# Kernel optimization log

Measured on AMD Instinct MI355X. Metric: run time of the kernel, lower is better.

The kernel has to match this reference:

```python
import jax, jax.numpy as jnp
import numpy as np

INC, ICS = 32, 8      # in_caps, in_caps_size
ONC, OCS = 32, 16     # out_caps, out_caps_size
K, STRIDE, PAD = 3, 1, 0
ITERS = 3


def squash(t, axis=-1):
    sq = jnp.sum(t * t, axis=axis, keepdims=True)
    return (sq / (1.0 + sq)) * t / jnp.sqrt(sq)


def setup_inputs() -> dict:
    key = jax.random.key(0)
    k1, k2 = jax.random.split(key)
    x = jax.random.normal(k1, (4, INC * ICS, 14, 14), dtype=jnp.float32)
    # nn.Parameter(torch.randn(...)); scaled by 1/sqrt(ICS) for numerical sanity
    weight = jax.random.normal(k2, (ONC, INC * K * K, ICS, OCS), dtype=jnp.float32) * (1.0 / np.sqrt(ICS))
    return {"x": x, "weight": weight}


def reference(x, weight):
    B, C, H, W = x.shape
    OH = (H + 2 * PAD - K) // STRIDE + 1
    OW = (W + 2 * PAD - K) // STRIDE + 1
    # Tile2d: extract KxK patches -> (B, C*K*K, OH, OW), channel order (C, kh, kw)
    patches = jax.lax.conv_general_dilated_patches(
        x, (K, K), (STRIDE, STRIDE), padding=((PAD, PAD), (PAD, PAD)))
    # (B, INC, ICS, K*K, OH*OW) -> (B, OH*OW, K*K, INC, ICS) -> (N, KK*INC, ICS)
    tiles = patches.reshape(B, INC, ICS, K * K, OH * OW)
    tiles = tiles.transpose(0, 4, 3, 1, 2).reshape(B * OH * OW, K * K * INC, ICS)

    # priors: (ONC, N, KKI, OCS)  == x[None,:,:,None,:] @ W[:,None]
    priors = jnp.einsum('nki,okic->onkc', tiles, weight)

    # dynamic routing; logits broadcast over OCS in the original (identical math)
    N = B * OH * OW
    KKI = K * K * INC
    logits = jnp.zeros((ONC, N, KKI, 1), dtype=priors.dtype)
    outputs = None
    for i in range(ITERS):
        probs = jax.nn.softmax(logits, axis=2)              # over KKI routes
        outputs = squash(jnp.sum(probs * priors, axis=2, keepdims=True))  # (ONC,N,1,OCS)
        if i != ITERS - 1:
            logits = logits + jnp.sum(priors * outputs, axis=-1, keepdims=True)

    # (ONC, N, OCS) -> (N, ONC, OCS) -> (B, ONC*OCS, OH, OW)
    out = outputs[:, :, 0, :].transpose(1, 0, 2)
    out = out.reshape(B, OH, OW, ONC * OCS).transpose(0, 3, 1, 2)
    return out
```

## Files before the change

kernel.cpp:

```cpp
#include <hip/hip_runtime.h>

static constexpr int OHW = 12, NSP = 144;

__global__ void build_T(const float* __restrict__ x, float4* __restrict__ T4) {
    const int g = blockIdx.x * 256 + threadIdx.x;
    const int n = g / 576;
    const int q = g - n * 576;
    const int r = q << 2;
    const int k = r >> 3;
    const int i0 = r & 7;
    const int ic = k & 31;
    const int kk = k >> 5;
    const int kh = kk / 3, kw = kk - kh * 3;
    const int b = n / NSP;
    const int rm = n - b * NSP;
    const int oh = rm / OHW, ow = rm - oh * OHW;
    const float* xp = x + (size_t)(b * 256 + ic * 8 + i0) * 196
                        + (oh + kh) * 14 + (ow + kw);
    float4 v;
    v.x = xp[0];
    v.y = xp[196];
    v.z = xp[392];
    v.w = xp[588];
    T4[g] = v;
}

__device__ __forceinline__ void fma4(float4& a, float s, const float4& w) {
    a.x = fmaf(s, w.x, a.x);
    a.y = fmaf(s, w.y, a.y);
    a.z = fmaf(s, w.z, a.z);
    a.w = fmaf(s, w.w, a.w);
}

__device__ __forceinline__ float4 shfl_xor4(const float4& v, int m) {
    float4 r;
    r.x = __shfl_xor(v.x, m);
    r.y = __shfl_xor(v.y, m);
    r.z = __shfl_xor(v.z, m);
    r.w = __shfl_xor(v.w, m);
    return r;
}

__device__ __forceinline__ void do_j(const float4* __restrict__ T4,
                                     const float4* __restrict__ W4,
                                     float4* __restrict__ Pl,
                                     int o, int nbase, int k, int cg,
                                     int g_local, int lane) {
    float4 w[8];
    const float4* wp = W4 + (size_t)(o * 288 + k) * 32 + cg;
    #pragma unroll
    for (int i = 0; i < 8; ++i) w[i] = wp[i * 4];
    #pragma unroll
    for (int nn = 0; nn < 4; ++nn) {
        const float4* tp = T4 + (size_t)(nbase + nn) * 576 + k * 2;
        const float4 t0 = tp[0];
        const float4 t1 = tp[1];
        float4 a = make_float4(0.f, 0.f, 0.f, 0.f);
        fma4(a, t0.x, w[0]); fma4(a, t0.y, w[1]);
        fma4(a, t0.z, w[2]); fma4(a, t0.w, w[3]);
        fma4(a, t1.x, w[4]); fma4(a, t1.y, w[5]);
        fma4(a, t1.z, w[6]); fma4(a, t1.w, w[7]);
        Pl[nn * 576 + g_local * 64 + lane] = a;
    }
}

__global__ __launch_bounds__(256, 4)
void caps_main(const float4* __restrict__ T4, const float4* __restrict__ W4,
               float* __restrict__ out) {
    __shared__ float4 Pl[4 * 9 * 64];
    const int tid = threadIdx.x;
    const int o = blockIdx.y;
    const int nbase = blockIdx.x * 4;
    const int cg = tid & 3;
    const int kg = tid >> 2;
    const int wv = tid >> 6;
    const int lane = tid & 63;

    float4 P[18];

    #pragma unroll
    for (int j = 0; j < 5; ++j) {
        const int k = kg + 64 * j;
        const int g = wv + 4 * j;
        if (k < 288 && g < 9)
            do_j(T4, W4, Pl, o, nbase, k, cg, g, lane);
    }
    __syncthreads();
    #pragma unroll
    for (int jj = 0; jj < 9; ++jj)
        P[jj] = Pl[wv * 576 + jj * 64 + lane];
    __syncthreads();
    #pragma unroll
    for (int j = 0; j < 5; ++j) {
        const int k = kg + 64 * j;
        const int g = wv + 4 * j;
        if (k < 288 && g >= 9)
            do_j(T4, W4, Pl, o, nbase, k, cg, g - 9, lane);
    }
    __syncthreads();
    #pragma unroll
    for (int jj = 9; jj < 18; ++jj)
        P[jj] = Pl[wv * 576 + (jj - 9) * 64 + lane];

    float lj[18];
    #pragma unroll
    for (int jj = 0; jj < 18; ++jj) lj[jj] = 0.f;
    float4 vq = make_float4(0.f, 0.f, 0.f, 0.f);

    #pragma unroll
    for (int it = 0; it < 3; ++it) {
        float4 svU = make_float4(0.f, 0.f, 0.f, 0.f);
        float S;
        if (it == 0) {
            #pragma unroll
            for (int jj = 0; jj < 18; ++jj) {
                svU.x += P[jj].x; svU.y += P[jj].y;
                svU.z += P[jj].z; svU.w += P[jj].w;
            }
            #pragma unroll
            for (int m = 4; m < 64; m <<= 1) {
                const float4 t = shfl_xor4(svU, m);
                svU.x += t.x; svU.y += t.y; svU.z += t.z; svU.w += t.w;
            }
            S = 288.0f;
        } else {
            S = 0.f;
            #pragma unroll
            for (int jj = 0; jj < 18; ++jj) {
                const float e = __expf(lj[jj]);
                S += e;
                fma4(svU, e, P[jj]);
            }
            #pragma unroll
            for (int m = 4; m < 64; m <<= 1) {
                const float4 t = shfl_xor4(svU, m);
                svU.x += t.x; svU.y += t.y; svU.z += t.z; svU.w += t.w;
                S += __shfl_xor(S, m);
            }
        }
        const float invS = __frcp_rn(S);
        float4 s;
        s.x = svU.x * invS; s.y = svU.y * invS;
        s.z = svU.z * invS; s.w = svU.w * invS;
        float sq = s.x * s.x + s.y * s.y + s.z * s.z + s.w * s.w;
        sq += __shfl_xor(sq, 1);
        sq += __shfl_xor(sq, 2);
        const float scale = __fsqrt_rn(sq) / (1.0f + sq);
        vq.x = s.x * scale; vq.y = s.y * scale;
        vq.z = s.z * scale; vq.w = s.w * scale;

        if (it < 2) {
            #pragma unroll
            for (int jj = 0; jj < 18; ++jj) {
                float d = P[jj].x * vq.x + P[jj].y * vq.y +
                          P[jj].z * vq.z + P[jj].w * vq.w;
                d += __shfl_xor(d, 1);
                d += __shfl_xor(d, 2);
                lj[jj] += d;
            }
        }
    }

    if ((lane >> 2) == 0) {
        const int n = nbase + wv;
        const int b = n / NSP;
        const int rm = n - b * NSP;
        float* op = out + (size_t)(b * 512 + o * 16 + cg * 4) * NSP + rm;
        op[0 * NSP] = vq.x;
        op[1 * NSP] = vq.y;
        op[2 * NSP] = vq.z;
        op[3 * NSP] = vq.w;
    }
}

extern "C" void kernel_launch(void* const* d_in, const int* in_sizes, int n_in,
                              void* d_out, int out_size, void* d_ws, size_t ws_size,
                              hipStream_t stream) {
    const float* x  = (const float*)d_in[0];
    const float* wt = (const float*)d_in[1];
    float* out = (float*)d_out;
    float4* T4 = (float4*)d_ws;

    build_T<<<dim3(576 * 576 / 256), 256, 0, stream>>>(x, T4);
    caps_main<<<dim3(144, 32), 256, 0, stream>>>(T4, (const float4*)wt, out);
}
```

Baseline: 123.6 us.

## Fuse patch extraction into routing kernel, reading input directly

Drops the separate build_T kernel that materialised the im2col tile buffer in workspace. The main kernel now reads the four adjacent output-width positions straight from x with an unaligned 4-wide vector load per input channel and computes the priors from them. This removes one kernel launch and a full write and read of the tile buffer. In exchange it relies on the four positions in a block sharing a row (12 is divisible by 4) and on unaligned vector loads.

After: 130.9 us. +5.9%, slower.

```diff
diff --git a/kernel.cpp b/kernel.cpp
--- a/kernel.cpp
+++ b/kernel.cpp
@@ -2,28 +2,7 @@
 
 static constexpr int OHW = 12, NSP = 144;
 
-__global__ void build_T(const float* __restrict__ x, float4* __restrict__ T4) {
-    const int g = blockIdx.x * 256 + threadIdx.x;
-    const int n = g / 576;
-    const int q = g - n * 576;
-    const int r = q << 2;
-    const int k = r >> 3;
-    const int i0 = r & 7;
-    const int ic = k & 31;
-    const int kk = k >> 5;
-    const int kh = kk / 3, kw = kk - kh * 3;
-    const int b = n / NSP;
-    const int rm = n - b * NSP;
-    const int oh = rm / OHW, ow = rm - oh * OHW;
-    const float* xp = x + (size_t)(b * 256 + ic * 8 + i0) * 196
-                        + (oh + kh) * 14 + (ow + kw);
-    float4 v;
-    v.x = xp[0];
-    v.y = xp[196];
-    v.z = xp[392];
-    v.w = xp[588];
-    T4[g] = v;
-}
+typedef float float4a __attribute__((ext_vector_type(4), aligned(4)));
 
 __device__ __forceinline__ void fma4(float4& a, float s, const float4& w) {
     a.x = fmaf(s, w.x, a.x);
@@ -41,32 +20,44 @@
     return r;
 }
 
-__device__ __forceinline__ void do_j(const float4* __restrict__ T4,
+__device__ __forceinline__ void do_j(const float* __restrict__ xb,
                                      const float4* __restrict__ W4,
                                      float4* __restrict__ Pl,
-                                     int o, int nbase, int k, int cg,
+                                     int o, int k, int cg,
                                      int g_local, int lane) {
     float4 w[8];
     const float4* wp = W4 + (size_t)(o * 288 + k) * 32 + cg;
     #pragma unroll
     for (int i = 0; i < 8; ++i) w[i] = wp[i * 4];
+
+    const int ic = k & 31;
+    const int kk = k >> 5;
+    const int kh = (kk * 11) >> 5;
+    const int kw = kk - 3 * kh;
+    const float* xp = xb + ic * (8 * 196) + kh * 14 + kw;
+
+    float4a v[8];
     #pragma unroll
-    for (int nn = 0; nn < 4; ++nn) {
-        const float4* tp = T4 + (size_t)(nbase + nn) * 576 + k * 2;
-        const float4 t0 = tp[0];
-        const float4 t1 = tp[1];
-        float4 a = make_float4(0.f, 0.f, 0.f, 0.f);
-        fma4(a, t0.x, w[0]); fma4(a, t0.y, w[1]);
-        fma4(a, t0.z, w[2]); fma4(a, t0.w, w[3]);
-        fma4(a, t1.x, w[4]); fma4(a, t1.y, w[5]);
-        fma4(a, t1.z, w[6]); fma4(a, t1.w, w[7]);
-        Pl[nn * 576 + g_local * 64 + lane] = a;
+    for (int i = 0; i < 8; ++i) v[i] = *(const float4a*)(xp + i * 196);
+
+    float4 acc[4];
+    #pragma unroll
+    for (int nn = 0; nn < 4; ++nn) acc[nn] = make_float4(0.f, 0.f, 0.f, 0.f);
+    #pragma unroll
+    for (int i = 0; i < 8; ++i) {
+        fma4(acc[0], v[i].x, w[i]);
+        fma4(acc[1], v[i].y, w[i]);
+        fma4(acc[2], v[i].z, w[i]);
+        fma4(acc[3], v[i].w, w[i]);
     }
+    #pragma unroll
+    for (int nn = 0; nn < 4; ++nn)
+        Pl[nn * 576 + g_local * 64 + lane] = acc[nn];
 }
 
 __global__ __launch_bounds__(256, 4)
-void caps_main(const float4* __restrict__ T4, const float4* __restrict__ W4,
-               float* __restrict__ out) {
+void caps_fused(const float* __restrict__ x, const float4* __restrict__ W4,
+                float* __restrict__ out) {
     __shared__ float4 Pl[4 * 9 * 64];
     const int tid = threadIdx.x;
     const int o = blockIdx.y;
@@ -76,6 +67,12 @@
     const int wv = tid >> 6;
     const int lane = tid & 63;
 
+    const int b = nbase / NSP;
+    const int rm = nbase - b * NSP;
+    const int oh = rm / OHW;
+    const int ow0 = rm - oh * OHW;
+    const float* xb = x + (size_t)b * (256 * 196) + oh * 14 + ow0;
+
     float4 P[18];
 
     #pragma unroll
@@ -83,7 +80,7 @@
         const int k = kg + 64 * j;
         const int g = wv + 4 * j;
         if (k < 288 && g < 9)
-            do_j(T4, W4, Pl, o, nbase, k, cg, g, lane);
+            do_j(xb, W4, Pl, o, k, cg, g, lane);
     }
     __syncthreads();
     #pragma unroll
@@ -95,7 +92,7 @@
         const int k = kg + 64 * j;
         const int g = wv + 4 * j;
         if (k < 288 && g >= 9)
-            do_j(T4, W4, Pl, o, nbase, k, cg, g - 9, lane);
+            do_j(xb, W4, Pl, o, k, cg, g - 9, lane);
     }
     __syncthreads();
     #pragma unroll
@@ -162,10 +159,7 @@
     }
 
     if ((lane >> 2) == 0) {
-        const int n = nbase + wv;
-        const int b = n / NSP;
-        const int rm = n - b * NSP;
-        float* op = out + (size_t)(b * 512 + o * 16 + cg * 4) * NSP + rm;
+        float* op = out + (size_t)(b * 512 + o * 16 + cg * 4) * NSP + (rm + wv);
         op[0 * NSP] = vq.x;
         op[1 * NSP] = vq.y;
         op[2 * NSP] = vq.z;
@@ -179,8 +173,5 @@
     const float* x  = (const float*)d_in[0];
     const float* wt = (const float*)d_in[1];
     float* out = (float*)d_out;
-    float4* T4 = (float4*)d_ws;
-
-    build_T<<<dim3(576 * 576 / 256), 256, 0, stream>>>(x, T4);
-    caps_main<<<dim3(144, 32), 256, 0, stream>>>(T4, (const float4*)wt, out);
+    caps_fused<<<dim3(144, 32), 256, 0, stream>>>(x, (const float4*)wt, out);
 }
```

## Split routing across two waves per position with 512-thread blocks

Applied to the files above, without the earlier changes.

Each capsule block now uses 512 threads, and each spatial position is handled by two wavefronts. Each wavefront holds 9 of the 18 prior float4s per lane, which halves per-thread register pressure and raises the launch bounds occupancy target. Partial routing sums and softmax denominators are combined across the wave pair through shared memory, at the cost of extra __syncthreads per routing iteration. Prior computation is redistributed so the two halves are produced in two phases over the same shared buffer.

After: 148.9 us. +20.5%, slower.

```diff
diff --git a/kernel.cpp b/kernel.cpp
--- a/kernel.cpp
+++ b/kernel.cpp
@@ -32,6 +32,10 @@
     a.w = fmaf(s, w.w, a.w);
 }
 
+__device__ __forceinline__ void add4(float4& a, const float4& b) {
+    a.x += b.x; a.y += b.y; a.z += b.z; a.w += b.w;
+}
+
 __device__ __forceinline__ float4 shfl_xor4(const float4& v, int m) {
     float4 r;
     r.x = __shfl_xor(v.x, m);
@@ -64,7 +68,7 @@
     }
 }
 
-__global__ __launch_bounds__(256, 4)
+__global__ __launch_bounds__(512, 6)
 void caps_main(const float4* __restrict__ T4, const float4* __restrict__ W4,
                float* __restrict__ out) {
     __shared__ float4 Pl[4 * 9 * 64];
@@ -72,39 +76,46 @@
     const int o = blockIdx.y;
     const int nbase = blockIdx.x * 4;
     const int cg = tid & 3;
-    const int kg = tid >> 2;
+    const int lane = tid & 63;
+    const int kgp = lane >> 2;
     const int wv = tid >> 6;
-    const int lane = tid & 63;
+    const int nl = wv >> 1;
+    const int khf = wv & 1;
 
-    float4 P[18];
+    do_j(T4, W4, Pl, o, nbase, kgp + 16 * wv, cg, wv, lane);
+    if (wv == 0)
+        do_j(T4, W4, Pl, o, nbase, kgp + 16 * 8, cg, 8, lane);
+    __syncthreads();
 
-    #pragma unroll
-    for (int j = 0; j < 5; ++j) {
-        const int k = kg + 64 * j;
-        const int g = wv + 4 * j;
-        if (k < 288 && g < 9)
-            do_j(T4, W4, Pl, o, nbase, k, cg, g, lane);
+    float4 P[9];
+    if (khf == 0) {
+        #pragma unroll
+        for (int jj = 0; jj < 9; ++jj)
+            P[jj] = Pl[nl * 576 + jj * 64 + lane];
     }
     __syncthreads();
-    #pragma unroll
-    for (int jj = 0; jj < 9; ++jj)
-        P[jj] = Pl[wv * 576 + jj * 64 + lane];
-    __syncthreads();
-    #pragma unroll
-    for (int j = 0; j < 5; ++j) {
-        const int k = kg + 64 * j;
-        const int g = wv + 4 * j;
-        if (k < 288 && g >= 9)
-            do_j(T4, W4, Pl, o, nbase, k, cg, g - 9, lane);
+
+    if (khf == 1) {
+        const int m = wv >> 1;
+        do_j(T4, W4, Pl, o, nbase, kgp + 16 * (9 + m),  cg, m,     lane);
+        do_j(T4, W4, Pl, o, nbase, kgp + 16 * (13 + m), cg, 4 + m, lane);
+        if (m == 0)
+            do_j(T4, W4, Pl, o, nbase, kgp + 16 * 17, cg, 8, lane);
     }
     __syncthreads();
+    if (khf == 1) {
+        #pragma unroll
+        for (int jj = 0; jj < 9; ++jj)
+            P[jj] = Pl[nl * 576 + jj * 64 + lane];
+    }
+    __syncthreads();
+
+    float4* xb4 = Pl;
+    float*  xbS = (float*)(Pl + 512);
+
+    float lj[9];
     #pragma unroll
-    for (int jj = 9; jj < 18; ++jj)
-        P[jj] = Pl[wv * 576 + (jj - 9) * 64 + lane];
-
-    float lj[18];
-    #pragma unroll
-    for (int jj = 0; jj < 18; ++jj) lj[jj] = 0.f;
+    for (int jj = 0; jj < 9; ++jj) lj[jj] = 0.f;
     float4 vq = make_float4(0.f, 0.f, 0.f, 0.f);
 
     #pragma unroll
@@ -113,20 +124,15 @@
         float S;
         if (it == 0) {
             #pragma unroll
-            for (int jj = 0; jj < 18; ++jj) {
-                svU.x += P[jj].x; svU.y += P[jj].y;
-                svU.z += P[jj].z; svU.w += P[jj].w;
-            }
+            for (int jj = 0; jj < 9; ++jj) add4(svU, P[jj]);
             #pragma unroll
-            for (int m = 4; m < 64; m <<= 1) {
-                const float4 t = shfl_xor4(svU, m);
-                svU.x += t.x; svU.y += t.y; svU.z += t.z; svU.w += t.w;
-            }
+            for (int m = 4; m < 64; m <<= 1)
+                { const float4 t = shfl_xor4(svU, m); add4(svU, t); }
             S = 288.0f;
         } else {
             S = 0.f;
             #pragma unroll
-            for (int jj = 0; jj < 18; ++jj) {
+            for (int jj = 0; jj < 9; ++jj) {
                 const float e = __expf(lj[jj]);
                 S += e;
                 fma4(svU, e, P[jj]);
@@ -134,10 +140,17 @@
             #pragma unroll
             for (int m = 4; m < 64; m <<= 1) {
                 const float4 t = shfl_xor4(svU, m);
-                svU.x += t.x; svU.y += t.y; svU.z += t.z; svU.w += t.w;
+                add4(svU, t);
                 S += __shfl_xor(S, m);
             }
         }
+        xb4[wv * 64 + lane] = svU;
+        if (it) xbS[wv * 64 + lane] = S;
+        __syncthreads();
+        add4(svU, xb4[(wv ^ 1) * 64 + lane]);
+        if (it) S += xbS[(wv ^ 1) * 64 + lane];
+        if (it < 2) __syncthreads();
+
         const float invS = __frcp_rn(S);
         float4 s;
         s.x = svU.x * invS; s.y = svU.y * invS;
@@ -151,7 +164,7 @@
 
         if (it < 2) {
             #pragma unroll
-            for (int jj = 0; jj < 18; ++jj) {
+            for (int jj = 0; jj < 9; ++jj) {
                 float d = P[jj].x * vq.x + P[jj].y * vq.y +
                           P[jj].z * vq.z + P[jj].w * vq.w;
                 d += __shfl_xor(d, 1);
@@ -161,8 +174,8 @@
         }
     }
 
-    if ((lane >> 2) == 0) {
-        const int n = nbase + wv;
+    if (khf == 0 && kgp == 0) {
+        const int n = nbase + nl;
         const int b = n / NSP;
         const int rm = n - b * NSP;
         float* op = out + (size_t)(b * 512 + o * 16 + cg * 4) * NSP + rm;
@@ -182,5 +195,5 @@
     float4* T4 = (float4*)d_ws;
 
     build_T<<<dim3(576 * 576 / 256), 256, 0, stream>>>(x, T4);
-    caps_main<<<dim3(144, 32), 256, 0, stream>>>(T4, (const float4*)wt, out);
+    caps_main<<<dim3(144, 32), 512, 0, stream>>>(T4, (const float4*)wt, out);
 }
```
